# Kernel optimization log

Measured on AMD Instinct MI355X. Metric: run time of the kernel, lower is better.

Reference implementation:

```python
import jax, jax.numpy as jnp
import numpy as np

NEG = -1.0e9
EPS = 1e-5

def layernorm(x, g, b):
    mu = jnp.mean(x, axis=-1, keepdims=True)
    var = jnp.mean((x - mu) ** 2, axis=-1, keepdims=True)
    return (x - mu) * jax.lax.rsqrt(var + EPS) * g + b

def setup_inputs() -> dict:
    key = jax.random.key(0)
    ks = jax.random.split(key, 20)
    B, S, D, H, F = 4, 2048, 1024, 16, 4096
    s = 0.02
    inp = {
        "x": jax.random.normal(ks[0], (B, S, D), jnp.float32),
        "attention_mask": jax.random.randint(ks[1], (B, S), 0, 2, jnp.int32),
        "Wq": jax.random.normal(ks[2], (D, D), jnp.float32) * s,
        "bq": jnp.zeros((D,), jnp.float32),
        "Wk": jax.random.normal(ks[3], (D, D), jnp.float32) * s,
        "bk": jnp.zeros((D,), jnp.float32),
        "Wv": jax.random.normal(ks[4], (D, D), jnp.float32) * s,
        "bv": jnp.zeros((D,), jnp.float32),
        "Wo": jax.random.normal(ks[5], (D, D), jnp.float32) * s,
        "bo": jnp.zeros((D,), jnp.float32),
        "W1": jax.random.normal(ks[6], (D, F), jnp.float32) * s,
        "b1": jnp.zeros((F,), jnp.float32),
        "W2": jax.random.normal(ks[7], (F, D), jnp.float32) * s,
        "b2": jnp.zeros((D,), jnp.float32),
        "g1": jnp.ones((D,), jnp.float32),
        "be1": jnp.zeros((D,), jnp.float32),
        "g2": jnp.ones((D,), jnp.float32),
        "be2": jnp.zeros((D,), jnp.float32),
    }
    return inp

def reference(x, Wq, bq, Wk, bk, Wv, bv, Wo, bo, W1, b1, W2, b2, g1, be1, g2, be2, attention_mask):
    B, S, D = x.shape
    H = 16
    dk = D // H

    # --- attention sublayer (pre-norm) ---
    h = layernorm(x, g1, be1)
    q = (h @ Wq + bq).reshape(B, S, H, dk).transpose(0, 2, 1, 3)  # (B,H,S,dk)
    k = (h @ Wk + bk).reshape(B, S, H, dk).transpose(0, 2, 1, 3)
    v = (h @ Wv + bv).reshape(B, S, H, dk).transpose(0, 2, 1, 3)

    scores = jnp.einsum("bhqd,bhkd->bhqk", q, k) / jnp.sqrt(jnp.float32(dk))
    causal = jnp.triu(jnp.ones((S, S), bool), k=1)  # True above diagonal
    scores = jnp.where(causal, NEG, scores)
    pad = (attention_mask == 0)[:, None, None, :]  # (B,1,1,S) key-side padding
    scores = jnp.where(pad, NEG, scores)

    attn = jax.nn.softmax(scores, axis=-1)
    attn = jnp.nan_to_num(attn, nan=0.0)
    ctx = jnp.einsum("bhqk,bhkd->bhqd", attn, v)
    ctx = ctx.transpose(0, 2, 1, 3).reshape(B, S, D)
    attn_out = ctx @ Wo + bo
    x = x + attn_out

    # --- FFN sublayer (pre-norm) ---
    h2 = layernorm(x, g2, be2)
    ffn = jax.nn.gelu(h2 @ W1 + b1, approximate=False) @ W2 + b2
    return x + ffn
```

## Files before the change

### kernel.cpp

```cpp
#include <hip/hip_runtime.h>
#include <math.h>


#define NEGV (-1.0e9f)

typedef short bfrag __attribute__((ext_vector_type(8)));
typedef float ffrag __attribute__((ext_vector_type(4)));
typedef unsigned short usvec8 __attribute__((ext_vector_type(8)));

__device__ __forceinline__ unsigned short f2bf(float f) {
  unsigned u = __float_as_uint(f);
  u += 0x7fffu + ((u >> 16) & 1u);
  return (unsigned short)(u >> 16);
}
__device__ __forceinline__ float bf2f(unsigned short h) {
  return __uint_as_float(((unsigned)h) << 16);
}
__device__ __forceinline__ float gelu_f(float v) {
  return 0.5f * v * (1.0f + erff(v * 0.7071067811865475f));
}
__device__ __forceinline__ void gload16(const void* g, void* l) {
  __builtin_amdgcn_global_load_lds(
      (const __attribute__((address_space(1))) void*)g,
      (__attribute__((address_space(3))) void*)l, 16, 0, 0);
}

__global__ __launch_bounds__(256) void transpose_cast(
    const float* __restrict__ src, unsigned short* __restrict__ dst,
    int R, int C) {
  __shared__ float tile[32][33];
  int bx = blockIdx.x, by = blockIdx.y;
  int tx = threadIdx.x & 31, ty = threadIdx.x >> 5;
#pragma unroll
  for (int i = 0; i < 4; ++i)
    tile[ty + i * 8][tx] =
        src[(size_t)(by * 32 + ty + i * 8) * C + bx * 32 + tx];
  __syncthreads();
#pragma unroll
  for (int i = 0; i < 4; ++i)
    dst[(size_t)(bx * 32 + ty + i * 8) * R + by * 32 + tx] =
        f2bf(tile[tx][ty + i * 8]);
}

__global__ __launch_bounds__(256) void bias_concat(
    const float* __restrict__ bq, const float* __restrict__ bk,
    const float* __restrict__ bv, float* __restrict__ dst) {
  int i = blockIdx.x * 256 + threadIdx.x;
  const float* src = (i < 1024) ? bq : (i < 2048 ? bk : bv);
  int off = (i < 1024) ? i : (i < 2048 ? i - 1024 : i - 2048);
  dst[i] = src[off];
}

__global__ __launch_bounds__(256) void ln_bf16(
    const float* __restrict__ X, const float* __restrict__ G,
    const float* __restrict__ Bt, unsigned short* __restrict__ O) {
  int row = blockIdx.x, t = threadIdx.x;
  const float* xr = X + (size_t)row * 1024;
  float4 x4 = *(const float4*)(xr + t * 4);
  float s = x4.x + x4.y + x4.z + x4.w;
#pragma unroll
  for (int off = 1; off < 64; off <<= 1) s += __shfl_xor(s, off);
  __shared__ float p1[4], p2[4];
  int wv = t >> 6, ln = t & 63;
  if (ln == 0) p1[wv] = s;
  __syncthreads();
  float mu = (p1[0] + p1[1] + p1[2] + p1[3]) * (1.0f / 1024.0f);
  float d0 = x4.x - mu, d1 = x4.y - mu, d2 = x4.z - mu, d3 = x4.w - mu;
  float q = d0 * d0 + d1 * d1 + d2 * d2 + d3 * d3;
#pragma unroll
  for (int off = 1; off < 64; off <<= 1) q += __shfl_xor(q, off);
  if (ln == 0) p2[wv] = q;
  __syncthreads();
  float var = (p2[0] + p2[1] + p2[2] + p2[3]) * (1.0f / 1024.0f);
  float rstd = rsqrtf(var + 1e-5f);
  float4 g4 = *(const float4*)(G + t * 4);
  float4 b4 = *(const float4*)(Bt + t * 4);
  ushort4 o4;
  o4.x = f2bf(d0 * rstd * g4.x + b4.x);
  o4.y = f2bf(d1 * rstd * g4.y + b4.y);
  o4.z = f2bf(d2 * rstd * g4.z + b4.z);
  o4.w = f2bf(d3 * rstd * g4.w + b4.w);
  *(ushort4*)(O + (size_t)row * 1024 + t * 4) = o4;
}

template <int DO_BIAS, int DO_RES, int DO_GELU, int OUT_BF16>
__global__ __launch_bounds__(256) void gemm_bf16(
    const unsigned short* __restrict__ A, const unsigned short* __restrict__ BT,
    const float* __restrict__ bias, const float* __restrict__ res,
    void* __restrict__ Cv, int M, int N, int K, int lda, int ldbt, int ldc) {
  __shared__ short Asm[128 * 64];
  __shared__ short Bsm[128 * 64];
  const int t = threadIdx.x;
  const int wv = t >> 6, lane = t & 63;
  const int wm = wv >> 1, wn = wv & 1;
  const int bn0 = blockIdx.x * 128, bm0 = blockIdx.y * 128;
  const int srow = t >> 3, sunit = t & 7;
  ffrag acc[4][4];
#pragma unroll
  for (int i = 0; i < 4; ++i)
#pragma unroll
    for (int j = 0; j < 4; ++j) acc[i][j] = {0.f, 0.f, 0.f, 0.f};

  for (int kk = 0; kk < K; kk += 64) {
#pragma unroll
    for (int i = 0; i < 4; ++i) {
      int row = i * 32 + srow;
      int su = sunit ^ (row & 7);
      gload16(A + (size_t)(bm0 + row) * lda + kk + su * 8,
              Asm + i * 2048 + wv * 512);
    }
#pragma unroll
    for (int i = 0; i < 4; ++i) {
      int row = i * 32 + srow;
      int su = sunit ^ (row & 7);
      gload16(BT + (size_t)(bn0 + row) * ldbt + kk + su * 8,
              Bsm + i * 2048 + wv * 512);
    }
    asm volatile("s_waitcnt vmcnt(0)" ::: "memory");
    __syncthreads();
#pragma unroll
    for (int kh = 0; kh < 2; ++kh) {
      bfrag af[4], bf[4];
#pragma unroll
      for (int mi = 0; mi < 4; ++mi) {
        int row = wm * 64 + mi * 16 + (lane & 15);
        int u = (kh * 4 + (lane >> 4)) ^ (row & 7);
        af[mi] = *(const bfrag*)&Asm[row * 64 + u * 8];
      }
#pragma unroll
      for (int ni = 0; ni < 4; ++ni) {
        int row = wn * 64 + ni * 16 + (lane & 15);
        int u = (kh * 4 + (lane >> 4)) ^ (row & 7);
        bf[ni] = *(const bfrag*)&Bsm[row * 64 + u * 8];
      }
#pragma unroll
      for (int mi = 0; mi < 4; ++mi)
#pragma unroll
        for (int ni = 0; ni < 4; ++ni)
          acc[mi][ni] = __builtin_amdgcn_mfma_f32_16x16x32_bf16(
              af[mi], bf[ni], acc[mi][ni], 0, 0, 0);
    }
    __syncthreads();
  }
  const int crow0 = bm0 + wm * 64 + (lane >> 4) * 4;
  const int ccol0 = bn0 + wn * 64 + (lane & 15);
#pragma unroll
  for (int ni = 0; ni < 4; ++ni) {
    int col = ccol0 + ni * 16;
    float bi = DO_BIAS ? bias[col] : 0.0f;
#pragma unroll
    for (int mi = 0; mi < 4; ++mi) {
#pragma unroll
      for (int r = 0; r < 4; ++r) {
        int row = crow0 + mi * 16 + r;
        float v = acc[mi][ni][r] + bi;
        if (DO_GELU) v = gelu_f(v);
        if (DO_RES) v += res[(size_t)row * ldc + col];
        if (OUT_BF16)
          ((unsigned short*)Cv)[(size_t)row * ldc + col] = f2bf(v);
        else
          ((float*)Cv)[(size_t)row * ldc + col] = v;
      }
    }
  }
}

__global__ __launch_bounds__(256) void vtrans(
    const unsigned short* __restrict__ V, unsigned short* __restrict__ VT,
    int ld) {
  __shared__ unsigned short tile[64 * 65];
  int st = blockIdx.x, bh = blockIdx.y;
  int b = bh >> 4, hh = bh & 15;
  int t = threadIdx.x;
  int s0 = st * 64;
  int sr = t >> 3, u = t & 7;
#pragma unroll
  for (int p = 0; p < 2; ++p) {
    int s = p * 32 + sr;
    usvec8 vv = *(const usvec8*)(V + (size_t)(b * 2048 + s0 + s) * ld +
                                 hh * 64 + u * 8);
#pragma unroll
    for (int j = 0; j < 8; ++j) tile[(u * 8 + j) * 65 + s] = vv[j];
  }
  __syncthreads();
  int dr = t >> 2, c = t & 3;
#pragma unroll
  for (int p = 0; p < 2; ++p) {
    int su = p * 4 + c;
    usvec8 ov;
#pragma unroll
    for (int j = 0; j < 8; ++j) ov[j] = tile[dr * 65 + su * 8 + j];
    *(usvec8*)(VT + (size_t)bh * 64 * 2048 + (size_t)dr * 2048 + s0 + su * 8) =
        ov;
  }
}

__global__ __launch_bounds__(256) void vsum_k(
    const unsigned short* __restrict__ VT, float* __restrict__ vsum) {
  int bh = blockIdx.x;
  int t = threadIdx.x;
  int d = t >> 2, c = t & 3;
  const unsigned short* row = VT + (size_t)bh * 131072 + (size_t)d * 2048;
  float acc = 0.0f;
#pragma unroll 4
  for (int i = 0; i < 64; ++i) {
    usvec8 vv = *(const usvec8*)(row + c * 8 + i * 32);
#pragma unroll
    for (int j = 0; j < 8; ++j) acc += bf2f(vv[j]);
  }
  acc += __shfl_xor(acc, 1);
  acc += __shfl_xor(acc, 2);
  if (c == 0) vsum[bh * 64 + d] = acc;
}

__global__ __launch_bounds__(256) void attn_mfma(
    const unsigned short* __restrict__ QKV, const unsigned short* __restrict__ VT,
    const int* __restrict__ amask, const float* __restrict__ vsum,
    unsigned short* __restrict__ ctx) {
  const int S = 2048, LD = 3072, D = 1024;
  int qt = blockIdx.x, hh = blockIdx.y, b = blockIdx.z;
  int t = threadIdx.x;
  int wv = t >> 6, lane = t & 63;
  int l15 = lane & 15, l4 = lane >> 4;
  __shared__ short Qs[64 * 64];
  __shared__ short Ks[2][64 * 64];
  __shared__ short Vs[2][64 * 64];
  __shared__ short Ps[4][16 * 64];
  const int srow = t >> 3, sunit = t & 7;

  const unsigned short* qb = QKV + (size_t)(b * S + qt * 64) * LD + hh * 64;
  const unsigned short* kbase = QKV + (size_t)b * S * LD + 1024 + hh * 64;
  const unsigned short* vtb = VT + (size_t)(b * 16 + hh) * 64 * 2048;

#pragma unroll
  for (int i = 0; i < 2; ++i) {
    int row = i * 32 + srow;
    int su = sunit ^ (row & 7);
    gload16(qb + (size_t)row * LD + su * 8, Qs + i * 2048 + wv * 512);
    gload16(kbase + (size_t)row * LD + su * 8, &Ks[0][i * 2048 + wv * 512]);
    gload16(vtb + (size_t)row * 2048 + su * 8, &Vs[0][i * 2048 + wv * 512]);
  }
  asm volatile("s_waitcnt vmcnt(0)" ::: "memory");
  __syncthreads();

  bfrag aq[2];
#pragma unroll
  for (int kh = 0; kh < 2; ++kh) {
    int row = wv * 16 + l15;
    int u = (kh * 4 + l4) ^ (row & 7);
    aq[kh] = *(const bfrag*)&Qs[row * 64 + u * 8];
  }

  ffrag o[4];
#pragma unroll
  for (int ni = 0; ni < 4; ++ni) o[ni] = {0.f, 0.f, 0.f, 0.f};
  float mrun[4] = {-INFINITY, -INFINITY, -INFINITY, -INFINITY};
  float lrun[4] = {0.f, 0.f, 0.f, 0.f};
  const int qrow0 = qt * 64 + wv * 16 + l4 * 4;
  int cur = 0;

  for (int kt = 0; kt <= qt; ++kt) {
    if (kt) {
      asm volatile("s_waitcnt vmcnt(0)" ::: "memory");
      __syncthreads();
    }
    if (kt < qt) {
#pragma unroll
      for (int i = 0; i < 2; ++i) {
        int row = i * 32 + srow;
        int su = sunit ^ (row & 7);
        gload16(kbase + (size_t)((kt + 1) * 64 + row) * LD + su * 8,
                &Ks[cur ^ 1][i * 2048 + wv * 512]);
        gload16(vtb + (size_t)row * 2048 + (kt + 1) * 64 + su * 8,
                &Vs[cur ^ 1][i * 2048 + wv * 512]);
      }
    }
    const short* ksb = Ks[cur];
    const short* vsb = Vs[cur];

    float sv[4][4];
#pragma unroll
    for (int ni = 0; ni < 4; ++ni) {
      ffrag sf = {0.f, 0.f, 0.f, 0.f};
#pragma unroll
      for (int kh = 0; kh < 2; ++kh) {
        int row = ni * 16 + l15;
        int u = (kh * 4 + l4) ^ (row & 7);
        bfrag bk = *(const bfrag*)&ksb[row * 64 + u * 8];
        sf = __builtin_amdgcn_mfma_f32_16x16x32_bf16(aq[kh], bk, sf, 0, 0, 0);
      }
#pragma unroll
      for (int r = 0; r < 4; ++r) sv[ni][r] = sf[r] * 0.125f;
    }
    if (kt == qt) {
#pragma unroll
      for (int ni = 0; ni < 4; ++ni) {
        int kpos = kt * 64 + ni * 16 + l15;
        int mk = amask[b * S + kpos];
#pragma unroll
        for (int r = 0; r < 4; ++r)
          if (mk == 0 || kpos > qrow0 + r) sv[ni][r] = NEGV;
      }
    } else {
#pragma unroll
      for (int ni = 0; ni < 4; ++ni) {
        int kpos = kt * 64 + ni * 16 + l15;
        int mk = amask[b * S + kpos];
        if (mk == 0) {
#pragma unroll
          for (int r = 0; r < 4; ++r) sv[ni][r] = NEGV;
        }
      }
    }
    float alpha[4];
#pragma unroll
    for (int r = 0; r < 4; ++r) {
      float mt = fmaxf(fmaxf(sv[0][r], sv[1][r]), fmaxf(sv[2][r], sv[3][r]));
#pragma unroll
      for (int off = 1; off < 16; off <<= 1) mt = fmaxf(mt, __shfl_xor(mt, off));
      float mn = fmaxf(mrun[r], mt);
      alpha[r] = __expf(mrun[r] - mn);
      float rs = 0.0f;
#pragma unroll
      for (int ni = 0; ni < 4; ++ni) {
        float pv = __expf(sv[ni][r] - mn);
        sv[ni][r] = pv;
        rs += pv;
      }
#pragma unroll
      for (int off = 1; off < 16; off <<= 1) rs += __shfl_xor(rs, off);
      lrun[r] = lrun[r] * alpha[r] + rs;
      mrun[r] = mn;
    }
#pragma unroll
    for (int ni = 0; ni < 4; ++ni) {
      int cu = ni * 2 + (l15 >> 3);
#pragma unroll
      for (int r = 0; r < 4; ++r) {
        int row = l4 * 4 + r;
        int su = cu ^ (row & 7);
        Ps[wv][row * 64 + su * 8 + (l15 & 7)] = f2bf(sv[ni][r]);
      }
    }
#pragma unroll
    for (int ni = 0; ni < 4; ++ni)
#pragma unroll
      for (int r = 0; r < 4; ++r) o[ni][r] *= alpha[r];
    bfrag pa[2];
#pragma unroll
    for (int kh = 0; kh < 2; ++kh) {
      int row = l15;
      int u = (kh * 4 + l4) ^ (row & 7);
      pa[kh] = *(const bfrag*)&Ps[wv][row * 64 + u * 8];
    }
#pragma unroll
    for (int ni = 0; ni < 4; ++ni) {
#pragma unroll
      for (int kh = 0; kh < 2; ++kh) {
        int drow = ni * 16 + l15;
        int u = (kh * 4 + l4) ^ (drow & 7);
        bfrag bv = *(const bfrag*)&vsb[drow * 64 + u * 8];
        o[ni] = __builtin_amdgcn_mfma_f32_16x16x32_bf16(pa[kh], bv, o[ni], 0, 0, 0);
      }
    }
    cur ^= 1;
  }
#pragma unroll
  for (int r = 0; r < 4; ++r) {
    float inv = 1.0f / lrun[r];
    bool allm = (mrun[r] <= -1.0e8f);
    int row_g = qrow0 + r;
#pragma unroll
    for (int ni = 0; ni < 4; ++ni) {
      float val;
      if (allm)
        val = vsum[(b * 16 + hh) * 64 + ni * 16 + l15] * (1.0f / 2048.0f);
      else
        val = o[ni][r] * inv;
      ctx[(size_t)(b * S + row_g) * D + hh * 64 + ni * 16 + l15] = f2bf(val);
    }
  }
}

extern "C" void kernel_launch(void* const* d_in, const int* in_sizes, int n_in,
                              void* d_out, int out_size, void* d_ws,
                              size_t ws_size, hipStream_t stream) {
  (void)in_sizes; (void)n_in; (void)out_size; (void)ws_size;
  const float* x   = (const float*)d_in[0];
  const int*   am  = (const int*)d_in[1];
  const float* Wq  = (const float*)d_in[2];
  const float* bq  = (const float*)d_in[3];
  const float* Wk  = (const float*)d_in[4];
  const float* bk  = (const float*)d_in[5];
  const float* Wv  = (const float*)d_in[6];
  const float* bv  = (const float*)d_in[7];
  const float* Wo  = (const float*)d_in[8];
  const float* bo  = (const float*)d_in[9];
  const float* W1  = (const float*)d_in[10];
  const float* b1  = (const float*)d_in[11];
  const float* W2  = (const float*)d_in[12];
  const float* b2  = (const float*)d_in[13];
  const float* g1  = (const float*)d_in[14];
  const float* be1 = (const float*)d_in[15];
  const float* g2  = (const float*)d_in[16];
  const float* be2 = (const float*)d_in[17];
  float* out = (float*)d_out;

  unsigned char* w8 = (unsigned char*)d_ws;
  const size_t MB = 1024ull * 1024;
  unsigned short* WqkvT = (unsigned short*)(w8 + 0 * MB);
  unsigned short* WoT   = (unsigned short*)(w8 + 6 * MB);
  unsigned short* W1T   = (unsigned short*)(w8 + 8 * MB);
  unsigned short* W2T   = (unsigned short*)(w8 + 16 * MB);
  unsigned short* h     = (unsigned short*)(w8 + 24 * MB);
  unsigned short* qkv   = (unsigned short*)(w8 + 40 * MB);
  unsigned short* vT    = (unsigned short*)(w8 + 88 * MB);
  float*          vsm   = (float*)(w8 + 104 * MB);
  float*          bqkv  = (float*)(w8 + 104 * MB + 16 * 1024);
  unsigned short* ctx = h;
  unsigned short* h2  = qkv;
  unsigned short* fc  = (unsigned short*)(w8 + 56 * MB);
  float*          x1  = out;

  bias_concat<<<12, 256, 0, stream>>>(bq, bk, bv, bqkv);
  transpose_cast<<<dim3(32, 32), 256, 0, stream>>>(Wq, WqkvT, 1024, 1024);
  transpose_cast<<<dim3(32, 32), 256, 0, stream>>>(Wk, WqkvT + 1024 * 1024, 1024, 1024);
  transpose_cast<<<dim3(32, 32), 256, 0, stream>>>(Wv, WqkvT + 2048 * 1024, 1024, 1024);
  transpose_cast<<<dim3(32, 32), 256, 0, stream>>>(Wo, WoT, 1024, 1024);
  transpose_cast<<<dim3(128, 32), 256, 0, stream>>>(W1, W1T, 1024, 4096);
  transpose_cast<<<dim3(32, 128), 256, 0, stream>>>(W2, W2T, 4096, 1024);

  ln_bf16<<<8192, 256, 0, stream>>>(x, g1, be1, h);
  gemm_bf16<1, 0, 0, 1><<<dim3(24, 64), 256, 0, stream>>>(
      h, WqkvT, bqkv, nullptr, qkv, 8192, 3072, 1024, 1024, 1024, 3072);
  vtrans<<<dim3(32, 64), 256, 0, stream>>>(qkv + 2048, vT, 3072);
  vsum_k<<<64, 256, 0, stream>>>(vT, vsm);
  attn_mfma<<<dim3(32, 16, 4), 256, 0, stream>>>(qkv, vT, am, vsm, ctx);
  gemm_bf16<1, 1, 0, 0><<<dim3(8, 64), 256, 0, stream>>>(
      ctx, WoT, bo, x, x1, 8192, 1024, 1024, 1024, 1024, 1024);
  ln_bf16<<<8192, 256, 0, stream>>>(x1, g2, be2, h2);
  for (int p = 0; p < 2; ++p) {
    gemm_bf16<1, 0, 1, 1><<<dim3(16, 64), 256, 0, stream>>>(
        h2, W1T + (size_t)p * 2048 * 1024, b1 + p * 2048, nullptr, fc,
        8192, 2048, 1024, 1024, 1024, 2048);
    if (p == 0) {
      gemm_bf16<1, 1, 0, 0><<<dim3(8, 64), 256, 0, stream>>>(
          fc, W2T + p * 2048, b2, x1, out, 8192, 1024, 2048, 2048, 4096, 1024);
    } else {
      gemm_bf16<0, 1, 0, 0><<<dim3(8, 64), 256, 0, stream>>>(
          fc, W2T + p * 2048, nullptr, out, out, 8192, 1024, 2048, 2048, 4096, 1024);
    }
  }
}
```

Baseline: 731.7 us.

## Process 128 query rows per attention block to reuse K/V tiles

Result: slower. 800.6 us (+9.4%).

```diff
diff --git a/kernel.cpp b/kernel.cpp
--- a/kernel.cpp
+++ b/kernel.cpp
@@ -222,49 +222,53 @@
   int t = threadIdx.x;
   int wv = t >> 6, lane = t & 63;
   int l15 = lane & 15, l4 = lane >> 4;
-  __shared__ short Qs[64 * 64];
   __shared__ short Ks[2][64 * 64];
   __shared__ short Vs[2][64 * 64];
-  __shared__ short Ps[4][16 * 64];
+  __shared__ short Ps[4][32 * 64];
   const int srow = t >> 3, sunit = t & 7;
 
-  const unsigned short* qb = QKV + (size_t)(b * S + qt * 64) * LD + hh * 64;
   const unsigned short* kbase = QKV + (size_t)b * S * LD + 1024 + hh * 64;
   const unsigned short* vtb = VT + (size_t)(b * 16 + hh) * 64 * 2048;
+
+  bfrag aq[2][2];
+#pragma unroll
+  for (int g = 0; g < 2; ++g) {
+    const unsigned short* qr =
+        QKV + (size_t)(b * S + qt * 128 + g * 64 + wv * 16 + l15) * LD + hh * 64;
+#pragma unroll
+    for (int kh = 0; kh < 2; ++kh)
+      aq[g][kh] = *(const bfrag*)(qr + (kh * 4 + l4) * 8);
+  }
 
 #pragma unroll
   for (int i = 0; i < 2; ++i) {
     int row = i * 32 + srow;
     int su = sunit ^ (row & 7);
-    gload16(qb + (size_t)row * LD + su * 8, Qs + i * 2048 + wv * 512);
     gload16(kbase + (size_t)row * LD + su * 8, &Ks[0][i * 2048 + wv * 512]);
     gload16(vtb + (size_t)row * 2048 + su * 8, &Vs[0][i * 2048 + wv * 512]);
   }
   asm volatile("s_waitcnt vmcnt(0)" ::: "memory");
   __syncthreads();
 
-  bfrag aq[2];
-#pragma unroll
-  for (int kh = 0; kh < 2; ++kh) {
-    int row = wv * 16 + l15;
-    int u = (kh * 4 + l4) ^ (row & 7);
-    aq[kh] = *(const bfrag*)&Qs[row * 64 + u * 8];
-  }
-
-  ffrag o[4];
-#pragma unroll
-  for (int ni = 0; ni < 4; ++ni) o[ni] = {0.f, 0.f, 0.f, 0.f};
-  float mrun[4] = {-INFINITY, -INFINITY, -INFINITY, -INFINITY};
-  float lrun[4] = {0.f, 0.f, 0.f, 0.f};
-  const int qrow0 = qt * 64 + wv * 16 + l4 * 4;
+  ffrag o[2][4];
+  float mrun[2][4], lrun[2][4];
+#pragma unroll
+  for (int g = 0; g < 2; ++g)
+#pragma unroll
+    for (int r = 0; r < 4; ++r) {
+      o[g][r] = {0.f, 0.f, 0.f, 0.f};
+      mrun[g][r] = -INFINITY;
+      lrun[g][r] = 0.f;
+    }
+  const int nkt = 2 * qt + 2;
   int cur = 0;
 
-  for (int kt = 0; kt <= qt; ++kt) {
+  for (int kt = 0; kt < nkt; ++kt) {
     if (kt) {
       asm volatile("s_waitcnt vmcnt(0)" ::: "memory");
       __syncthreads();
     }
-    if (kt < qt) {
+    if (kt + 1 < nkt) {
 #pragma unroll
       for (int i = 0; i < 2; ++i) {
         int row = i * 32 + srow;
@@ -278,81 +282,93 @@
     const short* ksb = Ks[cur];
     const short* vsb = Vs[cur];
 
-    float sv[4][4];
+    float sv[2][4][4];
 #pragma unroll
     for (int ni = 0; ni < 4; ++ni) {
-      ffrag sf = {0.f, 0.f, 0.f, 0.f};
+      ffrag sf0 = {0.f, 0.f, 0.f, 0.f}, sf1 = {0.f, 0.f, 0.f, 0.f};
 #pragma unroll
       for (int kh = 0; kh < 2; ++kh) {
         int row = ni * 16 + l15;
         int u = (kh * 4 + l4) ^ (row & 7);
         bfrag bk = *(const bfrag*)&ksb[row * 64 + u * 8];
-        sf = __builtin_amdgcn_mfma_f32_16x16x32_bf16(aq[kh], bk, sf, 0, 0, 0);
-      }
-#pragma unroll
-      for (int r = 0; r < 4; ++r) sv[ni][r] = sf[r] * 0.125f;
-    }
-    if (kt == qt) {
+        sf0 = __builtin_amdgcn_mfma_f32_16x16x32_bf16(aq[0][kh], bk, sf0, 0, 0, 0);
+        sf1 = __builtin_amdgcn_mfma_f32_16x16x32_bf16(aq[1][kh], bk, sf1, 0, 0, 0);
+      }
+#pragma unroll
+      for (int r = 0; r < 4; ++r) {
+        sv[0][ni][r] = sf0[r] * 0.125f;
+        sv[1][ni][r] = sf1[r] * 0.125f;
+      }
+    }
+    const bool diag = (kt >= 2 * qt);
+#pragma unroll
+    for (int ni = 0; ni < 4; ++ni) {
+      int kpos = kt * 64 + ni * 16 + l15;
+      int mk = amask[b * S + kpos];
+#pragma unroll
+      for (int g = 0; g < 2; ++g) {
+        int q0 = qt * 128 + g * 64 + wv * 16 + l4 * 4;
+        if (mk == 0) {
+#pragma unroll
+          for (int r = 0; r < 4; ++r) sv[g][ni][r] = NEGV;
+        } else if (diag) {
+#pragma unroll
+          for (int r = 0; r < 4; ++r)
+            if (kpos > q0 + r) sv[g][ni][r] = NEGV;
+        }
+      }
+    }
+    float alpha[2][4];
+#pragma unroll
+    for (int g = 0; g < 2; ++g)
+#pragma unroll
+      for (int r = 0; r < 4; ++r) {
+        float mt = fmaxf(fmaxf(sv[g][0][r], sv[g][1][r]),
+                         fmaxf(sv[g][2][r], sv[g][3][r]));
+#pragma unroll
+        for (int off = 1; off < 16; off <<= 1)
+          mt = fmaxf(mt, __shfl_xor(mt, off));
+        float mn = fmaxf(mrun[g][r], mt);
+        alpha[g][r] = __expf(mrun[g][r] - mn);
+        float rs = 0.0f;
+#pragma unroll
+        for (int ni = 0; ni < 4; ++ni) {
+          float pv = __expf(sv[g][ni][r] - mn);
+          sv[g][ni][r] = pv;
+          rs += pv;
+        }
+#pragma unroll
+        for (int off = 1; off < 16; off <<= 1) rs += __shfl_xor(rs, off);
+        lrun[g][r] = lrun[g][r] * alpha[g][r] + rs;
+        mrun[g][r] = mn;
+      }
+#pragma unroll
+    for (int g = 0; g < 2; ++g)
 #pragma unroll
       for (int ni = 0; ni < 4; ++ni) {
-        int kpos = kt * 64 + ni * 16 + l15;
-        int mk = amask[b * S + kpos];
-#pragma unroll
-        for (int r = 0; r < 4; ++r)
-          if (mk == 0 || kpos > qrow0 + r) sv[ni][r] = NEGV;
-      }
-    } else {
-#pragma unroll
-      for (int ni = 0; ni < 4; ++ni) {
-        int kpos = kt * 64 + ni * 16 + l15;
-        int mk = amask[b * S + kpos];
-        if (mk == 0) {
-#pragma unroll
-          for (int r = 0; r < 4; ++r) sv[ni][r] = NEGV;
+        int cu = ni * 2 + (l15 >> 3);
+#pragma unroll
+        for (int r = 0; r < 4; ++r) {
+          int row = g * 16 + l4 * 4 + r;
+          int su = cu ^ (row & 7);
+          Ps[wv][row * 64 + su * 8 + (l15 & 7)] = f2bf(sv[g][ni][r]);
         }
       }
-    }
-    float alpha[4];
-#pragma unroll
-    for (int r = 0; r < 4; ++r) {
-      float mt = fmaxf(fmaxf(sv[0][r], sv[1][r]), fmaxf(sv[2][r], sv[3][r]));
-#pragma unroll
-      for (int off = 1; off < 16; off <<= 1) mt = fmaxf(mt, __shfl_xor(mt, off));
-      float mn = fmaxf(mrun[r], mt);
-      alpha[r] = __expf(mrun[r] - mn);
-      float rs = 0.0f;
-#pragma unroll
-      for (int ni = 0; ni < 4; ++ni) {
-        float pv = __expf(sv[ni][r] - mn);
-        sv[ni][r] = pv;
-        rs += pv;
-      }
-#pragma unroll
-      for (int off = 1; off < 16; off <<= 1) rs += __shfl_xor(rs, off);
-      lrun[r] = lrun[r] * alpha[r] + rs;
-      mrun[r] = mn;
-    }
-#pragma unroll
-    for (int ni = 0; ni < 4; ++ni) {
-      int cu = ni * 2 + (l15 >> 3);
-#pragma unroll
-      for (int r = 0; r < 4; ++r) {
-        int row = l4 * 4 + r;
-        int su = cu ^ (row & 7);
-        Ps[wv][row * 64 + su * 8 + (l15 & 7)] = f2bf(sv[ni][r]);
-      }
-    }
-#pragma unroll
-    for (int ni = 0; ni < 4; ++ni)
-#pragma unroll
-      for (int r = 0; r < 4; ++r) o[ni][r] *= alpha[r];
-    bfrag pa[2];
-#pragma unroll
-    for (int kh = 0; kh < 2; ++kh) {
-      int row = l15;
-      int u = (kh * 4 + l4) ^ (row & 7);
-      pa[kh] = *(const bfrag*)&Ps[wv][row * 64 + u * 8];
-    }
+#pragma unroll
+    for (int g = 0; g < 2; ++g)
+#pragma unroll
+      for (int ni = 0; ni < 4; ++ni)
+#pragma unroll
+        for (int r = 0; r < 4; ++r) o[g][ni][r] *= alpha[g][r];
+    bfrag pa[2][2];
+#pragma unroll
+    for (int g = 0; g < 2; ++g)
+#pragma unroll
+      for (int kh = 0; kh < 2; ++kh) {
+        int row = g * 16 + l15;
+        int u = (kh * 4 + l4) ^ (row & 7);
+        pa[g][kh] = *(const bfrag*)&Ps[wv][row * 64 + u * 8];
+      }
 #pragma unroll
     for (int ni = 0; ni < 4; ++ni) {
 #pragma unroll
@@ -360,26 +376,29 @@
         int drow = ni * 16 + l15;
         int u = (kh * 4 + l4) ^ (drow & 7);
         bfrag bv = *(const bfrag*)&vsb[drow * 64 + u * 8];
-        o[ni] = __builtin_amdgcn_mfma_f32_16x16x32_bf16(pa[kh], bv, o[ni], 0, 0, 0);
+        o[0][ni] = __builtin_amdgcn_mfma_f32_16x16x32_bf16(pa[0][kh], bv, o[0][ni], 0, 0, 0);
+        o[1][ni] = __builtin_amdgcn_mfma_f32_16x16x32_bf16(pa[1][kh], bv, o[1][ni], 0, 0, 0);
       }
     }
     cur ^= 1;
   }
 #pragma unroll
-  for (int r = 0; r < 4; ++r) {
-    float inv = 1.0f / lrun[r];
-    bool allm = (mrun[r] <= -1.0e8f);
-    int row_g = qrow0 + r;
-#pragma unroll
-    for (int ni = 0; ni < 4; ++ni) {
-      float val;
-      if (allm)
-        val = vsum[(b * 16 + hh) * 64 + ni * 16 + l15] * (1.0f / 2048.0f);
-      else
-        val = o[ni][r] * inv;
-      ctx[(size_t)(b * S + row_g) * D + hh * 64 + ni * 16 + l15] = f2bf(val);
-    }
-  }
+  for (int g = 0; g < 2; ++g)
+#pragma unroll
+    for (int r = 0; r < 4; ++r) {
+      float inv = 1.0f / lrun[g][r];
+      bool allm = (mrun[g][r] <= -1.0e8f);
+      int row_g = qt * 128 + g * 64 + wv * 16 + l4 * 4 + r;
+#pragma unroll
+      for (int ni = 0; ni < 4; ++ni) {
+        float val;
+        if (allm)
+          val = vsum[(b * 16 + hh) * 64 + ni * 16 + l15] * (1.0f / 2048.0f);
+        else
+          val = o[g][ni][r] * inv;
+        ctx[(size_t)(b * S + row_g) * D + hh * 64 + ni * 16 + l15] = f2bf(val);
+      }
+    }
 }
 
 extern "C" void kernel_launch(void* const* d_in, const int* in_sizes, int n_in,
@@ -435,7 +454,7 @@
       h, WqkvT, bqkv, nullptr, qkv, 8192, 3072, 1024, 1024, 1024, 3072);
   vtrans<<<dim3(32, 64), 256, 0, stream>>>(qkv + 2048, vT, 3072);
   vsum_k<<<64, 256, 0, stream>>>(vT, vsm);
-  attn_mfma<<<dim3(32, 16, 4), 256, 0, stream>>>(qkv, vT, am, vsm, ctx);
+  attn_mfma<<<dim3(16, 16, 4), 256, 0, stream>>>(qkv, vT, am, vsm, ctx);
   gemm_bf16<1, 1, 0, 0><<<dim3(8, 64), 256, 0, stream>>>(
       ctx, WoT, bo, x, x1, 8192, 1024, 1024, 1024, 1024, 1024);
   ln_bf16<<<8192, 256, 0, stream>>>(x1, g2, be2, h2);
```
